# Performance work log

Hardware: AMD Instinct MI355X
Metric: run time of the kernel (lower is better)

Reference implementation:

```python
import jax, jax.numpy as jnp
import numpy as np

B, F, D = 1024, 256, 64  # batch, featureNumb, featureDim


def setup_inputs() -> dict:
    key = jax.random.key(0)
    k1, k2, k3, k4 = jax.random.split(key, 4)
    feature = jax.random.normal(k1, (B, F, D), dtype=jnp.float32)
    indicator = jax.random.normal(k2, (F, D), dtype=jnp.float32)
    # QKVTransformV2(n, D, D): n stacked DxD linear maps of the indicator
    W_qk = jax.random.normal(k3, (2, D, D), dtype=jnp.float32) / np.float32(np.sqrt(D))
    W_qkv = jax.random.normal(k4, (3, D, D), dtype=jnp.float32) / np.float32(np.sqrt(D))
    return {"feature": feature, "indicator": indicator, "W_qk": W_qk, "W_qkv": W_qkv}


def reference(feature, indicator, W_qk, W_qkv):
    d = indicator.shape[-1]
    scale = jnp.asarray(1.0 / np.sqrt(d), feature.dtype)

    # --- gate branch: QKTrans + DotWeight + LTE (straight-through hard threshold) ---
    trans = jnp.einsum('fd,nde->nfe', indicator, W_qk)            # [2,F,D]
    gate_logits = jnp.einsum('id,jd->ij', trans[0], trans[1]) * scale  # [F,F]
    gate = (gate_logits > 0).astype(feature.dtype)                # LTE forward: hard 0/1 gate

    # --- QKV branch, fused form of the rank-1 outer products ---
    # Original: QKV_outer[t,i,j] = qkv[t,i] (x) qkv[t,j]  (DxD rank-1)
    #           input[b,t,i,j,:] = feature[b,i] @ QKV_outer[t,i,j]
    #                            = (feature[b,i] . qkv[t,i]) * qkv[t,j]
    qkv = jnp.einsum('fd,nde->nfe', indicator, W_qkv)             # [3,F,D]
    s = jnp.einsum('bfd,nfd->nbf', feature, qkv)                  # s[t,b,i] = feature[b,i].qkv[t,i]

    # score[b,i,j] = input[b,0,i,j,:] . input[b,1,j,i,:]
    #              = s[0,b,i] * s[1,b,j] * (qkv[1,i] . qkv[0,j])
    cross = jnp.einsum('id,jd->ij', qkv[1], qkv[0])               # [F,F]
    score = s[0][:, :, None] * s[1][:, None, :] * cross[None]     # [B,F,F]
    scoreHat = score * gate[None]                                 # [B,F,F]

    # output[b,i,:] = sum_j scoreHat[b,i,j] * value[b,i,j,:]
    #               = s[2,b,i] * sum_j scoreHat[b,i,j] * qkv[2,j,:]
    out = s[2][:, :, None] * jnp.einsum('bij,jd->bid', scoreHat, qkv[2])  # [B,F,D]
    return out
```

## Files before the change

### kernel.cpp

```cpp
#include <hip/hip_runtime.h>
#include <stdint.h>

#define B 1024
#define F 256
#define D 64

typedef __attribute__((ext_vector_type(8))) short short8;
typedef __attribute__((ext_vector_type(4))) float f32x4;

__device__ __forceinline__ short f2bf(float f) {
    unsigned u = __builtin_bit_cast(unsigned, f);
    u += 0x7fff + ((u >> 16) & 1);
    return (short)(u >> 16);
}
__device__ __forceinline__ float bf2f(short s) {
    unsigned u = ((unsigned)(unsigned short)s) << 16;
    return __builtin_bit_cast(float, u);
}
__device__ __forceinline__ unsigned pk_bf16(float a, float b) {
    unsigned ua = __builtin_bit_cast(unsigned, a) + 0x8000u;
    unsigned ub = __builtin_bit_cast(unsigned, b) + 0x8000u;
    return __builtin_amdgcn_perm(ub, ua, 0x07060302u);
}


__global__ void precompute_trans(const float* __restrict__ indicator,
                                 const float* __restrict__ W_qk,
                                 const float* __restrict__ W_qkv,
                                 float* __restrict__ trans,
                                 float* __restrict__ qkv) {
    int idx = blockIdx.x * blockDim.x + threadIdx.x;
    int n   = idx / (F * D);
    int rem = idx - n * (F * D);
    int f   = rem / D;
    int e   = rem - f * D;
    const float* W = (n < 2) ? (W_qk + n * D * D) : (W_qkv + (n - 2) * D * D);
    const float* ind = indicator + f * D;
    float acc = 0.f;
#pragma unroll 8
    for (int d = 0; d < D; ++d) acc += ind[d] * W[d * D + e];
    if (n < 2) trans[n * F * D + f * D + e] = acc;
    else       qkv[(n - 2) * F * D + f * D + e] = acc;
}

__global__ __launch_bounds__(256) void compute_Mt(const float* __restrict__ trans,
                                                  const float* __restrict__ qkv,
                                                  short* __restrict__ At,
                                                  short* __restrict__ q2K) {
    int j = blockIdx.x;
    int i = threadIdx.x;
    const float4* t0 = (const float4*)(trans + i * D);
    const float4* t1 = (const float4*)(trans + F * D + j * D);
    const float4* q1 = (const float4*)(qkv + F * D + i * D);
    const float4* q0 = (const float4*)(qkv + j * D);
    float d0 = 0.f, d1 = 0.f;
#pragma unroll
    for (int k = 0; k < D / 4; ++k) {
        float4 a = t0[k], b = t1[k], c = q1[k], e = q0[k];
        d0 += a.x * b.x + a.y * b.y + a.z * b.z + a.w * b.w;
        d1 += c.x * e.x + c.y * e.y + c.z * e.z + c.w * e.w;
    }
    float v = (d0 > 0.f) ? d1 : 0.f;
    At[((j >> 5) * F + i) * 32 + (j & 31)] = f2bf(v);
    if (j < D) q2K[((i >> 5) * D + j) * 32 + (i & 31)] = f2bf(qkv[2 * F * D + i * D + j]);
}

__global__ __launch_bounds__(256, 2) void fused_main(const float* __restrict__ feature,
                                                     const float* __restrict__ qkv,
                                                     const short* __restrict__ At,
                                                     const short* __restrict__ q2K,
                                                     float* __restrict__ out) {
    int bp = blockIdx.x;
    int b0 = bp * 2;
    int tid = threadIdx.x;

    __shared__ __align__(16) short s1L[2 * F];
    __shared__ float gL[2 * F];

    {
        int rg = tid >> 4;
        int l  = tid & 15;
#pragma unroll 4
        for (int p = 0; p < 16; ++p) {
            int f = p * 16 + rg;
            float4 fv0 = ((const float4*)(feature + ((size_t)(b0 * F + f)) * D))[l];
            float4 fv1 = ((const float4*)(feature + ((size_t)((b0 + 1) * F + f)) * D))[l];
            float4 q0 = ((const float4*)(qkv + f * D))[l];
            float4 q1 = ((const float4*)(qkv + F * D + f * D))[l];
            float4 q2 = ((const float4*)(qkv + 2 * F * D + f * D))[l];
            float a00 = fv0.x * q0.x + fv0.y * q0.y + fv0.z * q0.z + fv0.w * q0.w;
            float a01 = fv0.x * q1.x + fv0.y * q1.y + fv0.z * q1.z + fv0.w * q1.w;
            float a02 = fv0.x * q2.x + fv0.y * q2.y + fv0.z * q2.z + fv0.w * q2.w;
            float a10 = fv1.x * q0.x + fv1.y * q0.y + fv1.z * q0.z + fv1.w * q0.w;
            float a11 = fv1.x * q1.x + fv1.y * q1.y + fv1.z * q1.z + fv1.w * q1.w;
            float a12 = fv1.x * q2.x + fv1.y * q2.y + fv1.z * q2.z + fv1.w * q2.w;
#pragma unroll
            for (int m = 1; m < 16; m <<= 1) {
                a00 += __shfl_xor(a00, m, 64);
                a01 += __shfl_xor(a01, m, 64);
                a02 += __shfl_xor(a02, m, 64);
                a10 += __shfl_xor(a10, m, 64);
                a11 += __shfl_xor(a11, m, 64);
                a12 += __shfl_xor(a12, m, 64);
            }
            if (l == 0) {
                gL[f]       = a00 * a02;
                gL[F + f]   = a10 * a12;
                s1L[f]      = f2bf(a01);
                s1L[F + f]  = f2bf(a11);
            }
        }
    }
    __syncthreads();

    int wave = tid >> 6;
    int lane = tid & 63;
    int wr   = wave >> 1, wc = wave & 1;
    int l16  = lane & 15;
    int lq   = lane >> 4;
    int kq   = lq * 8;
    int b    = b0 + wc;

    f32x4 acc[8][4];
#pragma unroll
    for (int mt = 0; mt < 8; ++mt)
#pragma unroll
        for (int nt = 0; nt < 4; ++nt) acc[mt][nt] = (f32x4){0.f, 0.f, 0.f, 0.f};

    for (int jt = 0; jt < F / 32; ++jt) {
        short8 sv = *(const short8*)(s1L + wc * F + jt * 32 + kq);
        float sf[8];
#pragma unroll
        for (int e = 0; e < 8; ++e) sf[e] = bf2f(sv[e]);

        short8 bfr[4];
#pragma unroll
        for (int nt = 0; nt < 4; ++nt) {
            int d = nt * 16 + l16;
            short8 qv = *(const short8*)(q2K + (jt * D + d) * 32 + kq);
            int4 packed;
            packed.x = pk_bf16(bf2f(qv[0]) * sf[0], bf2f(qv[1]) * sf[1]);
            packed.y = pk_bf16(bf2f(qv[2]) * sf[2], bf2f(qv[3]) * sf[3]);
            packed.z = pk_bf16(bf2f(qv[4]) * sf[4], bf2f(qv[5]) * sf[5]);
            packed.w = pk_bf16(bf2f(qv[6]) * sf[6], bf2f(qv[7]) * sf[7]);
            bfr[nt] = __builtin_bit_cast(short8, packed);
        }
#pragma unroll
        for (int mt = 0; mt < 8; ++mt) {
            int i = wr * 128 + mt * 16 + l16;
            short8 af = *(const short8*)(At + ((size_t)jt * F + i) * 32 + kq);
#pragma unroll
            for (int nt = 0; nt < 4; ++nt)
                acc[mt][nt] = __builtin_amdgcn_mfma_f32_16x16x32_bf16(
                    af, bfr[nt], acc[mt][nt], 0, 0, 0);
        }
    }

#pragma unroll
    for (int mt = 0; mt < 8; ++mt) {
#pragma unroll
        for (int r = 0; r < 4; ++r) {
            int i = wr * 128 + mt * 16 + lq * 4 + r;
            float gg = gL[wc * F + i];
            float* orow = out + ((size_t)(b * F + i)) * D;
#pragma unroll
            for (int nt = 0; nt < 4; ++nt)
                orow[nt * 16 + l16] = gg * acc[mt][nt][r];
        }
    }
}

extern "C" void kernel_launch(void* const* d_in, const int* in_sizes, int n_in,
                              void* d_out, int out_size, void* d_ws, size_t ws_size,
                              hipStream_t stream) {
    const float* feature   = (const float*)d_in[0];
    const float* indicator = (const float*)d_in[1];
    const float* W_qk      = (const float*)d_in[2];
    const float* W_qkv     = (const float*)d_in[3];
    float* out = (float*)d_out;

    float* ws    = (float*)d_ws;
    float* trans = ws;
    float* qkv   = trans + 2 * F * D;
    short* At    = (short*)(qkv + 3 * F * D);
    short* q2K   = At + F * F;

    hipLaunchKernelGGL(precompute_trans, dim3((5 * F * D) / 256), dim3(256), 0,
                       stream, indicator, W_qk, W_qkv, trans, qkv);
    hipLaunchKernelGGL(compute_Mt, dim3(F), dim3(F), 0, stream, trans, qkv, At, q2K);
    hipLaunchKernelGGL(fused_main, dim3(B / 2), dim3(256), 0, stream,
                       feature, qkv, At, q2K, out);
}
```

Measured before the change: 143.1 us.

## Process one batch per block with four waves splitting rows

Switches fused_main from handling two batch elements per 256-thread block to one batch per block. The four waves now each own 64 output rows instead of 128, so the accumulator array halves and the grid doubles to B blocks. Launch bounds are raised to allow four blocks per CU, aiming for higher occupancy and better latency hiding. The cost is that At and q2K are re-read by twice as many blocks, and the B-fragment scaling work per MFMA doubles relative to the A tiles.

Result: slower. 158.2 us (+10.5%).

```diff
diff --git a/kernel.cpp b/kernel.cpp
--- a/kernel.cpp
+++ b/kernel.cpp
@@ -65,17 +65,16 @@
     if (j < D) q2K[((i >> 5) * D + j) * 32 + (i & 31)] = f2bf(qkv[2 * F * D + i * D + j]);
 }
 
-__global__ __launch_bounds__(256, 2) void fused_main(const float* __restrict__ feature,
+__global__ __launch_bounds__(256, 4) void fused_main(const float* __restrict__ feature,
                                                      const float* __restrict__ qkv,
                                                      const short* __restrict__ At,
                                                      const short* __restrict__ q2K,
                                                      float* __restrict__ out) {
-    int bp = blockIdx.x;
-    int b0 = bp * 2;
+    int b   = blockIdx.x;
     int tid = threadIdx.x;
 
-    __shared__ __align__(16) short s1L[2 * F];
-    __shared__ float gL[2 * F];
+    __shared__ __align__(16) short s1L[F];
+    __shared__ float gL[F];
 
     {
         int rg = tid >> 4;
@@ -83,31 +82,22 @@
 #pragma unroll 4
         for (int p = 0; p < 16; ++p) {
             int f = p * 16 + rg;
-            float4 fv0 = ((const float4*)(feature + ((size_t)(b0 * F + f)) * D))[l];
-            float4 fv1 = ((const float4*)(feature + ((size_t)((b0 + 1) * F + f)) * D))[l];
+            float4 fv = ((const float4*)(feature + ((size_t)(b * F + f)) * D))[l];
             float4 q0 = ((const float4*)(qkv + f * D))[l];
             float4 q1 = ((const float4*)(qkv + F * D + f * D))[l];
             float4 q2 = ((const float4*)(qkv + 2 * F * D + f * D))[l];
-            float a00 = fv0.x * q0.x + fv0.y * q0.y + fv0.z * q0.z + fv0.w * q0.w;
-            float a01 = fv0.x * q1.x + fv0.y * q1.y + fv0.z * q1.z + fv0.w * q1.w;
-            float a02 = fv0.x * q2.x + fv0.y * q2.y + fv0.z * q2.z + fv0.w * q2.w;
-            float a10 = fv1.x * q0.x + fv1.y * q0.y + fv1.z * q0.z + fv1.w * q0.w;
-            float a11 = fv1.x * q1.x + fv1.y * q1.y + fv1.z * q1.z + fv1.w * q1.w;
-            float a12 = fv1.x * q2.x + fv1.y * q2.y + fv1.z * q2.z + fv1.w * q2.w;
+            float a0 = fv.x * q0.x + fv.y * q0.y + fv.z * q0.z + fv.w * q0.w;
+            float a1 = fv.x * q1.x + fv.y * q1.y + fv.z * q1.z + fv.w * q1.w;
+            float a2 = fv.x * q2.x + fv.y * q2.y + fv.z * q2.z + fv.w * q2.w;
 #pragma unroll
             for (int m = 1; m < 16; m <<= 1) {
-                a00 += __shfl_xor(a00, m, 64);
-                a01 += __shfl_xor(a01, m, 64);
-                a02 += __shfl_xor(a02, m, 64);
-                a10 += __shfl_xor(a10, m, 64);
-                a11 += __shfl_xor(a11, m, 64);
-                a12 += __shfl_xor(a12, m, 64);
+                a0 += __shfl_xor(a0, m, 64);
+                a1 += __shfl_xor(a1, m, 64);
+                a2 += __shfl_xor(a2, m, 64);
             }
             if (l == 0) {
-                gL[f]       = a00 * a02;
-                gL[F + f]   = a10 * a12;
-                s1L[f]      = f2bf(a01);
-                s1L[F + f]  = f2bf(a11);
+                gL[f]  = a0 * a2;
+                s1L[f] = f2bf(a1);
             }
         }
     }
@@ -115,20 +105,18 @@
 
     int wave = tid >> 6;
     int lane = tid & 63;
-    int wr   = wave >> 1, wc = wave & 1;
     int l16  = lane & 15;
     int lq   = lane >> 4;
     int kq   = lq * 8;
-    int b    = b0 + wc;
 
-    f32x4 acc[8][4];
+    f32x4 acc[4][4];
 #pragma unroll
-    for (int mt = 0; mt < 8; ++mt)
+    for (int mt = 0; mt < 4; ++mt)
 #pragma unroll
         for (int nt = 0; nt < 4; ++nt) acc[mt][nt] = (f32x4){0.f, 0.f, 0.f, 0.f};
 
     for (int jt = 0; jt < F / 32; ++jt) {
-        short8 sv = *(const short8*)(s1L + wc * F + jt * 32 + kq);
+        short8 sv = *(const short8*)(s1L + jt * 32 + kq);
         float sf[8];
 #pragma unroll
         for (int e = 0; e < 8; ++e) sf[e] = bf2f(sv[e]);
@@ -146,8 +134,8 @@
             bfr[nt] = __builtin_bit_cast(short8, packed);
         }
 #pragma unroll
-        for (int mt = 0; mt < 8; ++mt) {
-            int i = wr * 128 + mt * 16 + l16;
+        for (int mt = 0; mt < 4; ++mt) {
+            int i = wave * 64 + mt * 16 + l16;
             short8 af = *(const short8*)(At + ((size_t)jt * F + i) * 32 + kq);
 #pragma unroll
             for (int nt = 0; nt < 4; ++nt)
@@ -157,11 +145,11 @@
     }
 
 #pragma unroll
-    for (int mt = 0; mt < 8; ++mt) {
+    for (int mt = 0; mt < 4; ++mt) {
 #pragma unroll
         for (int r = 0; r < 4; ++r) {
-            int i = wr * 128 + mt * 16 + lq * 4 + r;
-            float gg = gL[wc * F + i];
+            int i = wave * 64 + mt * 16 + lq * 4 + r;
+            float gg = gL[i];
             float* orow = out + ((size_t)(b * F + i)) * D;
 #pragma unroll
             for (int nt = 0; nt < 4; ++nt)
@@ -188,6 +176,6 @@
     hipLaunchKernelGGL(precompute_trans, dim3((5 * F * D) / 256), dim3(256), 0,
                        stream, indicator, W_qk, W_qkv, trans, qkv);
     hipLaunchKernelGGL(compute_Mt, dim3(F), dim3(F), 0, stream, trans, qkv, At, q2K);
-    hipLaunchKernelGGL(fused_main, dim3(B / 2), dim3(256), 0, stream,
+    hipLaunchKernelGGL(fused_main, dim3(B), dim3(256), 0, stream,
                        feature, qkv, At, q2K, out);
 }
```
